# Optimization experiments

Measured on AMD Instinct MI355X. Metric: run time of the kernel, lower is better.

## Reference

```python
import math
import jax, jax.numpy as jnp
import numpy as np

B, S, H, D = 2, 8192, 16, 128
W = 4  # conv_kernel_size


def setup_inputs() -> dict:
    key = jax.random.key(0)
    ks = jax.random.split(key, 5)
    return {
        "q": jax.random.normal(ks[0], (B, S, H * D), dtype=jnp.float32),
        "k": jax.random.normal(ks[1], (B, S, H * D), dtype=jnp.float32),
        "v": jax.random.normal(ks[2], (B, S, H * D), dtype=jnp.float32),
        "a": jax.random.normal(ks[3], (B, S, H), dtype=jnp.float32),
        "b": jax.random.normal(ks[4], (B, S, H), dtype=jnp.float32),
        "head_dim": D,
        "conv_kernel_size": W,
    }


def reference(q, k, v, a, b, head_dim, conv_kernel_size):
    batch, seq_len, _ = q.shape
    kv_heads = k.shape[-1] // head_dim
    qh = q.reshape(batch, seq_len, kv_heads, head_dim)
    kh = k.reshape(batch, seq_len, kv_heads, head_dim)
    vh = v.reshape(batch, seq_len, kv_heads, head_dim)
    ah = a.reshape(batch, seq_len, kv_heads, 1)
    bh = b.reshape(batch, seq_len, kv_heads, 1)
    scale = 1.0 / math.sqrt(head_dim)

    out = jnp.zeros_like(vh)
    # For each offset delta, j = i - delta; padded (j<0) positions have k=v=0,
    # so their contribution (q.k)*gate*v is exactly zero.
    for delta in range(conv_kernel_size + 1):
        pad = ((0, 0), (delta, 0), (0, 0), (0, 0))
        kd = jnp.pad(kh, pad)[:, :seq_len]
        vd = jnp.pad(vh, pad)[:, :seq_len]
        bd = jnp.pad(bh, pad)[:, :seq_len]
        w = jnp.sum(qh * kd, axis=-1, keepdims=True) * scale  # [B,S,H,1]
        g = jax.nn.sigmoid(ah * bd)
        out = out + w * g * vd
    # position 0 is special-cased in the original: output = v_0 (no attention)
    out = out.at[:, 0].set(vh[:, 0])
    return out.reshape(batch, seq_len, -1)
```

## Files before the change

### kernel.cpp

```cpp
#include <hip/hip_runtime.h>
#include <math.h>

constexpr int B = 2;
constexpr int S = 8192;
constexpr int H = 16;
constexpr int D = 128;
constexpr int W = 4;
constexpr float SCALE = 0.08838834764831845f;

template <int CTRL>
__device__ __forceinline__ float dpp_xadd(float x) {
    int r = __builtin_amdgcn_update_dpp(0, __float_as_int(x), CTRL, 0xF, 0xF, false);
    return x + __int_as_float(r);
}

__device__ __forceinline__ float group_reduce32(float p) {
    p = dpp_xadd<0xB1>(p);
    p = dpp_xadd<0x4E>(p);
    p = dpp_xadd<0x141>(p);
    p = dpp_xadd<0x140>(p);
    int t = __builtin_amdgcn_ds_swizzle(__float_as_int(p), 0x401F);
    return p + __int_as_float(t);
}

__global__ __launch_bounds__(256) void gdr_kernel(
    const float* __restrict__ q, const float* __restrict__ k,
    const float* __restrict__ v, const float* __restrict__ a,
    const float* __restrict__ b, float* __restrict__ out)
{
    const int tid   = threadIdx.x;
    const int group = tid >> 5;
    const int lane  = tid & 31;

    const int bid = blockIdx.x;
    const int xcd = bid & 7;
    const int j   = bid >> 3;
    const int c   = j & 127;
    const int bh  = j >> 7;
    const int h   = bh & (H - 1);
    const int bb  = bh >> 4;

    const int s = xcd * (S / 8) + c * 8 + group;
    const long long bs = (long long)bb * S + s;

    const long long rowBase = bs * (long long)(H * D) + (long long)h * D;
    const int d0 = lane * 4;

    if (s == 0) {
        const float4 v4 = *(const float4*)(v + rowBase + d0);
        *(float4*)(out + rowBase + d0) = v4;
        return;
    }

    const float4 q4 = *(const float4*)(q + rowBase + d0);
    const float ai  = a[bs * H + h];
    float4 acc = make_float4(0.f, 0.f, 0.f, 0.f);

#pragma unroll
    for (int delta = 0; delta <= W; ++delta) {
        const int jj = s - delta;
        if (jj < 0) continue;
        const long long jBase = rowBase - (long long)delta * (H * D);
        const float4 k4 = *(const float4*)(k + jBase + d0);
        const float4 v4 = *(const float4*)(v + jBase + d0);

        float p = q4.x * k4.x + q4.y * k4.y + q4.z * k4.z + q4.w * k4.w;
        p = group_reduce32(p);

        const float bj = b[(bs - (long long)delta) * H + h];
        const float g  = 1.0f / (1.0f + __expf(-(ai * bj)));
        const float wg = p * SCALE * g;
        acc.x += wg * v4.x;
        acc.y += wg * v4.y;
        acc.z += wg * v4.z;
        acc.w += wg * v4.w;
    }

    *(float4*)(out + rowBase + d0) = acc;
}

extern "C" void kernel_launch(void* const* d_in, const int* in_sizes, int n_in,
                              void* d_out, int out_size, void* d_ws, size_t ws_size,
                              hipStream_t stream) {
    const float* q = (const float*)d_in[0];
    const float* k = (const float*)d_in[1];
    const float* v = (const float*)d_in[2];
    const float* a = (const float*)d_in[3];
    const float* b = (const float*)d_in[4];
    float* out = (float*)d_out;

    const int nRows = B * S * H;
    const int blocks = nRows / 8;
    gdr_kernel<<<blocks, 256, 0, stream>>>(q, k, v, a, b, out);
}
```

Before: 405.5 us.

## Slide a 5-row register window over 16 consecutive positions per group

Each 32-lane group now walks 16 consecutive sequence positions for one head. It keeps the last five k/v/b rows in a register ring buffer, so each k and v row is loaded once instead of up to five times. Blocks are remapped so that the eight groups cover eight heads, and q is prescaled. This cuts redundant global and L2 traffic but uses more registers per thread and launches far fewer blocks (launch bounds raised to request 5 waves per SIMD), which lowers parallelism.

After: 415.8 us. +2.5%, slower.

```diff
diff --git a/kernel.cpp b/kernel.cpp
--- a/kernel.cpp
+++ b/kernel.cpp
@@ -6,6 +6,8 @@
 constexpr int H = 16;
 constexpr int D = 128;
 constexpr int W = 4;
+constexpr int HD = H * D;
+constexpr int C = 16;
 constexpr float SCALE = 0.08838834764831845f;
 
 template <int CTRL>
@@ -23,7 +25,7 @@
     return p + __int_as_float(t);
 }
 
-__global__ __launch_bounds__(256) void gdr_kernel(
+__global__ __launch_bounds__(256, 5) void gdr_kernel(
     const float* __restrict__ q, const float* __restrict__ k,
     const float* __restrict__ v, const float* __restrict__ a,
     const float* __restrict__ b, float* __restrict__ out)
@@ -34,49 +36,74 @@
 
     const int bid = blockIdx.x;
     const int xcd = bid & 7;
-    const int j   = bid >> 3;
-    const int c   = j & 127;
-    const int bh  = j >> 7;
-    const int h   = bh & (H - 1);
-    const int bb  = bh >> 4;
+    int r = bid >> 3;
+    const int cw = r & 63;  r >>= 6;
+    const int hh = r & 1;
+    const int bb = r >> 1;
+    const int h  = hh * 8 + group;
+    const int s0 = xcd * (S / 8) + cw * C;
 
-    const int s = xcd * (S / 8) + c * 8 + group;
-    const long long bs = (long long)bb * S + s;
+    const int d0 = lane * 4;
+    const int eBase = ((bb * S + s0) * H + h) * D + d0;
+    const int rBase = (bb * S + s0) * H + h;
 
-    const long long rowBase = bs * (long long)(H * D) + (long long)h * D;
-    const int d0 = lane * 4;
-
-    if (s == 0) {
-        const float4 v4 = *(const float4*)(v + rowBase + d0);
-        *(float4*)(out + rowBase + d0) = v4;
-        return;
+    float4 kw[5], vw[5];
+    float  bw[5];
+    if (s0 != 0) {
+#pragma unroll
+        for (int i = 0; i < 4; ++i) {
+            const int e = eBase - (4 - i) * HD;
+            kw[i] = *(const float4*)(k + e);
+            vw[i] = *(const float4*)(v + e);
+            bw[i] = b[rBase - (4 - i) * H];
+        }
+    } else {
+#pragma unroll
+        for (int i = 0; i < 4; ++i) {
+            kw[i] = make_float4(0.f, 0.f, 0.f, 0.f);
+            vw[i] = make_float4(0.f, 0.f, 0.f, 0.f);
+            bw[i] = 0.f;
+        }
     }
 
-    const float4 q4 = *(const float4*)(q + rowBase + d0);
-    const float ai  = a[bs * H + h];
-    float4 acc = make_float4(0.f, 0.f, 0.f, 0.f);
+#pragma unroll
+    for (int st = 0; st < C; ++st) {
+        const int e   = eBase + st * HD;
+        const int rb  = rBase + st * H;
+        const int cur = (st + 4) % 5;
 
+        kw[cur] = *(const float4*)(k + e);
+        vw[cur] = *(const float4*)(v + e);
+        bw[cur] = b[rb];
+        float4 q4 = *(const float4*)(q + e);
+        const float ai = a[rb];
+        q4.x *= SCALE; q4.y *= SCALE; q4.z *= SCALE; q4.w *= SCALE;
+
+        float p[W + 1];
 #pragma unroll
-    for (int delta = 0; delta <= W; ++delta) {
-        const int jj = s - delta;
-        if (jj < 0) continue;
-        const long long jBase = rowBase - (long long)delta * (H * D);
-        const float4 k4 = *(const float4*)(k + jBase + d0);
-        const float4 v4 = *(const float4*)(v + jBase + d0);
+        for (int dl = 0; dl <= W; ++dl) {
+            const int sl = (st + 4 - dl) % 5;
+            float pp = q4.x * kw[sl].x + q4.y * kw[sl].y +
+                       q4.z * kw[sl].z + q4.w * kw[sl].w;
+            p[dl] = group_reduce32(pp);
+        }
 
-        float p = q4.x * k4.x + q4.y * k4.y + q4.z * k4.z + q4.w * k4.w;
-        p = group_reduce32(p);
+        float4 acc = make_float4(0.f, 0.f, 0.f, 0.f);
+#pragma unroll
+        for (int dl = 0; dl <= W; ++dl) {
+            const int sl = (st + 4 - dl) % 5;
+            const float g  = 1.0f / (1.0f + __expf(-(ai * bw[sl])));
+            const float wg = p[dl] * g;
+            acc.x += wg * vw[sl].x;
+            acc.y += wg * vw[sl].y;
+            acc.z += wg * vw[sl].z;
+            acc.w += wg * vw[sl].w;
+        }
 
-        const float bj = b[(bs - (long long)delta) * H + h];
-        const float g  = 1.0f / (1.0f + __expf(-(ai * bj)));
-        const float wg = p * SCALE * g;
-        acc.x += wg * v4.x;
-        acc.y += wg * v4.y;
-        acc.z += wg * v4.z;
-        acc.w += wg * v4.w;
+        float4 res = acc;
+        if (s0 + st == 0) res = vw[cur];
+        *(float4*)(out + e) = res;
     }
-
-    *(float4*)(out + rowBase + d0) = acc;
 }
 
 extern "C" void kernel_launch(void* const* d_in, const int* in_sizes, int n_in,
@@ -89,7 +116,6 @@
     const float* b = (const float*)d_in[4];
     float* out = (float*)d_out;
 
-    const int nRows = B * S * H;
-    const int blocks = nRows / 8;
+    const int blocks = B * 2 * 8 * (S / 8 / C);
     gdr_kernel<<<blocks, 256, 0, stream>>>(q, k, v, a, b, out);
 }
```

## Map one block per token with 16 lanes per head and batched loads

Applied to the files above, without the earlier changes.

Each block now handles one sequence position across all 16 heads, with 16 lanes per head each holding two float4 slices. That makes the dot-product reduction DPP-only and drops the ds_swizzle. All five k/v rows and gates are loaded up front for non-boundary positions to raise memory-level parallelism. The kernel also uses a hardware reciprocal and sets a launch-bounds occupancy hint. The trade-off is higher register pressure, and the grid mapping is rewritten.

Result: slower. 421.8 us (+4.0%).

```diff
diff --git a/kernel.cpp b/kernel.cpp
--- a/kernel.cpp
+++ b/kernel.cpp
@@ -6,6 +6,7 @@
 constexpr int H = 16;
 constexpr int D = 128;
 constexpr int W = 4;
+constexpr int HD = H * D;
 constexpr float SCALE = 0.08838834764831845f;
 
 template <int CTRL>
@@ -14,69 +15,97 @@
     return x + __int_as_float(r);
 }
 
-__device__ __forceinline__ float group_reduce32(float p) {
+__device__ __forceinline__ float group_reduce16(float p) {
     p = dpp_xadd<0xB1>(p);
     p = dpp_xadd<0x4E>(p);
     p = dpp_xadd<0x141>(p);
     p = dpp_xadd<0x140>(p);
-    int t = __builtin_amdgcn_ds_swizzle(__float_as_int(p), 0x401F);
-    return p + __int_as_float(t);
+    return p;
 }
 
-__global__ __launch_bounds__(256) void gdr_kernel(
+__device__ __forceinline__ float dot8(const float4& qa, const float4& qb,
+                                      const float4& ka, const float4& kb) {
+    return qa.x * ka.x + qa.y * ka.y + qa.z * ka.z + qa.w * ka.w +
+           qb.x * kb.x + qb.y * kb.y + qb.z * kb.z + qb.w * kb.w;
+}
+
+__global__ __launch_bounds__(256, 4) void gdr_kernel(
     const float* __restrict__ q, const float* __restrict__ k,
     const float* __restrict__ v, const float* __restrict__ a,
     const float* __restrict__ b, float* __restrict__ out)
 {
-    const int tid   = threadIdx.x;
-    const int group = tid >> 5;
-    const int lane  = tid & 31;
+    const int tid  = threadIdx.x;
+    const int h    = tid >> 4;
+    const int lane = tid & 15;
 
     const int bid = blockIdx.x;
     const int xcd = bid & 7;
     const int j   = bid >> 3;
-    const int c   = j & 127;
-    const int bh  = j >> 7;
-    const int h   = bh & (H - 1);
-    const int bb  = bh >> 4;
+    const int c   = j & 1023;
+    const int bb  = j >> 10;
+    const int s   = xcd * (S / 8) + c;
 
-    const int s = xcd * (S / 8) + c * 8 + group;
-    const long long bs = (long long)bb * S + s;
-
-    const long long rowBase = bs * (long long)(H * D) + (long long)h * D;
-    const int d0 = lane * 4;
+    const int bs  = bb * S + s;
+    const int row = bs * H + h;
+    const int e   = row * D + lane * 4;
 
     if (s == 0) {
-        const float4 v4 = *(const float4*)(v + rowBase + d0);
-        *(float4*)(out + rowBase + d0) = v4;
+        *(float4*)(out + e)      = *(const float4*)(v + e);
+        *(float4*)(out + e + 64) = *(const float4*)(v + e + 64);
         return;
     }
 
-    const float4 q4 = *(const float4*)(q + rowBase + d0);
-    const float ai  = a[bs * H + h];
-    float4 acc = make_float4(0.f, 0.f, 0.f, 0.f);
+    const float4 qa = *(const float4*)(q + e);
+    const float4 qb = *(const float4*)(q + e + 64);
+    const float  ai = a[row];
 
+    float4 acca = make_float4(0.f, 0.f, 0.f, 0.f);
+    float4 accb = make_float4(0.f, 0.f, 0.f, 0.f);
+
+    if (s >= W) {
+        float4 ka[W + 1], kb[W + 1], va[W + 1], vb[W + 1];
+        float  bg[W + 1];
 #pragma unroll
-    for (int delta = 0; delta <= W; ++delta) {
-        const int jj = s - delta;
-        if (jj < 0) continue;
-        const long long jBase = rowBase - (long long)delta * (H * D);
-        const float4 k4 = *(const float4*)(k + jBase + d0);
-        const float4 v4 = *(const float4*)(v + jBase + d0);
-
-        float p = q4.x * k4.x + q4.y * k4.y + q4.z * k4.z + q4.w * k4.w;
-        p = group_reduce32(p);
-
-        const float bj = b[(bs - (long long)delta) * H + h];
-        const float g  = 1.0f / (1.0f + __expf(-(ai * bj)));
-        const float wg = p * SCALE * g;
-        acc.x += wg * v4.x;
-        acc.y += wg * v4.y;
-        acc.z += wg * v4.z;
-        acc.w += wg * v4.w;
+        for (int d = 0; d <= W; ++d) {
+            const int ee = e - d * HD;
+            ka[d] = *(const float4*)(k + ee);
+            kb[d] = *(const float4*)(k + ee + 64);
+            va[d] = *(const float4*)(v + ee);
+            vb[d] = *(const float4*)(v + ee + 64);
+            bg[d] = b[row - d * H];
+        }
+#pragma unroll
+        for (int d = 0; d <= W; ++d) {
+            float p = dot8(qa, qb, ka[d], kb[d]);
+            p = group_reduce16(p);
+            const float g  = __builtin_amdgcn_rcpf(1.0f + __expf(-(ai * bg[d])));
+            const float wg = p * SCALE * g;
+            acca.x += wg * va[d].x; acca.y += wg * va[d].y;
+            acca.z += wg * va[d].z; acca.w += wg * va[d].w;
+            accb.x += wg * vb[d].x; accb.y += wg * vb[d].y;
+            accb.z += wg * vb[d].z; accb.w += wg * vb[d].w;
+        }
+    } else {
+        for (int d = 0; d <= s; ++d) {
+            const int ee = e - d * HD;
+            const float4 k4a = *(const float4*)(k + ee);
+            const float4 k4b = *(const float4*)(k + ee + 64);
+            const float4 v4a = *(const float4*)(v + ee);
+            const float4 v4b = *(const float4*)(v + ee + 64);
+            float p = dot8(qa, qb, k4a, k4b);
+            p = group_reduce16(p);
+            const float bj = b[row - d * H];
+            const float g  = __builtin_amdgcn_rcpf(1.0f + __expf(-(ai * bj)));
+            const float wg = p * SCALE * g;
+            acca.x += wg * v4a.x; acca.y += wg * v4a.y;
+            acca.z += wg * v4a.z; acca.w += wg * v4a.w;
+            accb.x += wg * v4b.x; accb.y += wg * v4b.y;
+            accb.z += wg * v4b.z; accb.w += wg * v4b.w;
+        }
     }
 
-    *(float4*)(out + rowBase + d0) = acc;
+    *(float4*)(out + e)      = acca;
+    *(float4*)(out + e + 64) = accb;
 }
 
 extern "C" void kernel_launch(void* const* d_in, const int* in_sizes, int n_in,
@@ -89,7 +118,6 @@
     const float* b = (const float*)d_in[4];
     float* out = (float*)d_out;
 
-    const int nRows = B * S * H;
-    const int blocks = nRows / 8;
+    const int blocks = B * S;
     gdr_kernel<<<blocks, 256, 0, stream>>>(q, k, v, a, b, out);
 }
```
